# Performance work log

Hardware: AMD Instinct MI355X
Metric: run time of the kernel (lower is better)

## Reference

```python
import jax, jax.numpy as jnp
import numpy as np

T_ITERS = 10
EPS = 1e-5


def setup_inputs() -> dict:
    key = jax.random.key(0)
    B, C, H, W = 64, 256, 56, 56
    X = jax.random.normal(key, (B, C, H, W), dtype=jnp.float32)
    # running_rot buffer: orthogonal rotation per group (g=1)
    M = np.random.default_rng(0).standard_normal((C, C)).astype(np.float32)
    q, _ = np.linalg.qr(M)
    running_rot = jnp.asarray(q[None, :, :])  # [g=1, d, d]
    return {"X": X, "running_rot": running_rot}


def _whiten(X, g, nc):
    # X: [B, C, H, W] -> x: [g, d, m] with m = B*H*W (training-mode IterNorm)
    B, C, H, W = X.shape
    x = jnp.transpose(X, (1, 0, 2, 3)).reshape(g, nc, -1)
    m = x.shape[-1]
    mean = jnp.mean(x, axis=-1, keepdims=True)          # [g, d, 1]
    xc = x - mean                                        # [g, d, m]
    I = jnp.broadcast_to(jnp.eye(nc, dtype=X.dtype), (g, nc, nc))
    Sigma = EPS * I + jnp.matmul(xc, jnp.swapaxes(xc, 1, 2)) * (1.0 / m)
    # rTr = 1 / trace(Sigma) per group
    rTr = 1.0 / jnp.sum(Sigma * I, axis=(1, 2), keepdims=True)  # [g,1,1]
    Sigma_N = Sigma * rTr
    # Newton-Schulz iteration: P_{k+1} = 1.5 P_k - 0.5 P_k^3 Sigma_N
    P = I
    for _ in range(T_ITERS):
        P3 = jnp.matmul(jnp.matmul(P, P), P)
        P = 1.5 * P - 0.5 * jnp.matmul(P3, Sigma_N)
    wm = P * jnp.sqrt(rTr)                               # whitening matrix [g,d,d]
    xn = jnp.matmul(wm, xc)                              # [g, d, m]
    return xn.reshape(C, B, H, W).transpose(1, 0, 2, 3)  # back to [B,C,H,W]


def reference(X, running_rot):
    g, _, nc = running_rot.shape
    B, C, H, W = X.shape
    X_hat = _whiten(X, g, nc)                            # [B, C, H, W]
    Xg = X_hat.reshape(B, g, nc, H, W)
    # rotate whitened features: Q^T alignment, einsum('bgchw,gdc->bgdhw')
    Xr = jnp.einsum('bgchw,gdc->bgdhw', Xg, running_rot)
    return Xr.reshape(B, C, H, W)
```

## Files before the change

### kernel.cpp

```cpp
#include <hip/hip_runtime.h>
#include <math.h>

#define HWn   3136
#define Cn    256
#define KCPB  49
#define NCHUNK 3136
#define INV_M (1.0f/200704.0f)
#define EPSc  1e-5f

typedef __attribute__((ext_vector_type(4))) float f32x4;
typedef __attribute__((ext_vector_type(8))) short s16x8;
typedef __attribute__((ext_vector_type(4))) unsigned short u16x4;

static __device__ __forceinline__ unsigned short f2bf(float f) {
  unsigned int u = __builtin_bit_cast(unsigned int, f);
  u = (u + 0x7fffu + ((u >> 16) & 1u)) >> 16;
  return (unsigned short)u;
}

static __device__ __forceinline__ unsigned int cvt_pk_bf16(float lo, float hi) {
  unsigned int r;
  asm("v_cvt_pk_bf16_f32 %0, %1, %2" : "=v"(r) : "v"(lo), "v"(hi));
  return r;
}

__global__ __launch_bounds__(1024) void k_gram(const float* __restrict__ X,
                                               float* __restrict__ Gp,
                                               float* __restrict__ Sp,
                                               float* __restrict__ Dp,
                                               int nparts) {
  __shared__ __align__(16) unsigned short lds[2][256 * 64];
  const int t = threadIdx.x, p = blockIdx.x;
  const int w = t >> 6, l = t & 63, a = l & 15, g = l >> 4;
  const int swzA = (a & 7) << 3;
  const int crow = t >> 4, sg = t & 15;

  f32x4 acc[16];
#pragma unroll
  for (int j = 0; j < 16; ++j) acc[j] = (f32x4){0.f, 0.f, 0.f, 0.f};
  float sum4[4] = {0.f, 0.f, 0.f, 0.f};
  float vx[16];

  const int start = (int)(((long)NCHUNK * p) / nparts);
  const int end   = (int)(((long)NCHUNK * (p + 1)) / nparts);

#define G_LOADS(CH)                                                           \
  {                                                                           \
    const int b_ = (CH) / KCPB, kc_ = (CH) % KCPB;                            \
    const float* xb_ = X + (long)b_ * Cn * HWn + kc_ * 64;                    \
    _Pragma("unroll")                                                         \
    for (int p4 = 0; p4 < 4; ++p4) {                                          \
      const float4 v = *(const float4*)(xb_ + (long)(p4 * 64 + crow) * HWn + sg * 4); \
      vx[p4 * 4 + 0] = v.x; vx[p4 * 4 + 1] = v.y;                             \
      vx[p4 * 4 + 2] = v.z; vx[p4 * 4 + 3] = v.w;                             \
    }                                                                         \
  }

#define G_CVTWR(BUF)                                                          \
  {                                                                           \
    _Pragma("unroll")                                                         \
    for (int p4 = 0; p4 < 4; ++p4) {                                          \
      const int c_ = p4 * 64 + crow;                                          \
      sum4[p4] += (vx[p4 * 4 + 0] + vx[p4 * 4 + 1])                           \
                + (vx[p4 * 4 + 2] + vx[p4 * 4 + 3]);                          \
      uint2 hh;                                                               \
      hh.x = cvt_pk_bf16(vx[p4 * 4 + 0], vx[p4 * 4 + 1]);                     \
      hh.y = cvt_pk_bf16(vx[p4 * 4 + 2], vx[p4 * 4 + 3]);                     \
      *(uint2*)(&lds[BUF][0] + ((c_ * 64 + sg * 4) ^ ((c_ & 7) << 3))) = hh;  \
    }                                                                         \
  }

  G_LOADS(start);
  G_CVTWR(0);
  __syncthreads();

  for (int ch = start; ch < end; ++ch) {
    const int cur = (ch - start) & 1;
    if (ch + 1 < end) G_LOADS(ch + 1);
    const unsigned short* tile = &lds[cur][0];
#pragma unroll
    for (int kk = 0; kk < 64; kk += 32) {
      const s16x8 fw = *(const s16x8*)(tile + (((w * 16 + a) * 64 + kk + g * 8) ^ swzA));
#pragma unroll
      for (int j = 0; j < 16; ++j) {
        const s16x8 fj = *(const s16x8*)(tile + (((j * 16 + a) * 64 + kk + g * 8) ^ swzA));
        acc[j] = __builtin_amdgcn_mfma_f32_16x16x32_bf16(fw, fj, acc[j], 0, 0, 0);
      }
    }
    if (ch + 1 < end) G_CVTWR(cur ^ 1);
    __syncthreads();
  }
#undef G_LOADS
#undef G_CVTWR

  float* gout = Gp + (long)p * 65536;
#pragma unroll
  for (int j = 0; j < 16; ++j)
#pragma unroll
    for (int r = 0; r < 4; ++r)
      __builtin_nontemporal_store(acc[j][r],
          gout + (16 * w + 4 * g + r) * 256 + 16 * j + a);

#pragma unroll
  for (int p4 = 0; p4 < 4; ++p4) {
    float s = sum4[p4];
    s += __shfl_xor(s, 1);
    s += __shfl_xor(s, 2);
    s += __shfl_xor(s, 4);
    s += __shfl_xor(s, 8);
    if (a == 0) Sp[(long)p * 256 + p4 * 64 + w * 4 + g] = s;
  }

  {
    float dsum = 0.f;
#pragma unroll
    for (int j = 0; j < 16; ++j) {
      if (j == w && (a >> 2) == g) {
#pragma unroll
        for (int r = 0; r < 4; ++r)
          if ((a & 3) == r) dsum = acc[j][r];
      }
    }
#pragma unroll
    for (int off = 1; off < 64; off <<= 1) dsum += __shfl_xor(dsum, off);
    float* lf = (float*)lds;
    if (l == 0) lf[w] = dsum;
    __syncthreads();
    if (t == 0) {
      float d = 0.f;
#pragma unroll
      for (int ww = 0; ww < 16; ++ww) d += lf[ww];
      Dp[p] = d;
    }
  }
}

__global__ __launch_bounds__(1024) void k_reduce(const float* __restrict__ Gp,
                                                 const float* __restrict__ Sp,
                                                 const float* __restrict__ Dp,
                                                 float* __restrict__ Sigma,
                                                 float* __restrict__ P1,
                                                 float* __restrict__ meansum,
                                                 float* __restrict__ scal,
                                                 int nparts) {
  __shared__ float redA[4][256];
  __shared__ float msh[256];
  __shared__ float scrD[256];
  __shared__ float scrM[256];
  __shared__ __align__(16) float redB[16][256];
  const int t = threadIdx.x, j = blockIdx.x;
  const int c = t & 255, g = t >> 8;

  {
    float s = 0.f;
    const int pa0 = (nparts * g) >> 2, pa1 = (nparts * (g + 1)) >> 2;
    for (int p = pa0; p < pa1; ++p) s += Sp[(long)p * 256 + c];
    redA[g][c] = s;
  }
  __syncthreads();
  if (g == 0) msh[c] = (redA[0][c] + redA[1][c]) + (redA[2][c] + redA[3][c]);
  __syncthreads();

  if (t < 256) {
    scrD[t] = (t < nparts) ? Dp[t] : 0.f;
    const float mc = msh[t] * INV_M;
    scrM[t] = mc * mc;
  }
  __syncthreads();
  for (int st = 128; st > 0; st >>= 1) {
    if (t < st) { scrD[t] += scrD[t + st]; scrM[t] += scrM[t + st]; }
    __syncthreads();
  }
  const float tr = scrD[0] * INV_M - scrM[0] + 256.f * EPSc;
  const float rTr = 1.0f / tr;

  {
    const int c4 = (t & 63) * 4, sl = t >> 6;
    const int pb0 = (nparts * sl) >> 4, pb1 = (nparts * (sl + 1)) >> 4;
    const float* gp = Gp + (long)pb0 * 65536 + (long)j * 256 + c4;
    f32x4 s4 = (f32x4){0.f, 0.f, 0.f, 0.f};
    for (int p = pb0; p < pb1; ++p) {
      s4 += __builtin_nontemporal_load((const f32x4*)gp);
      gp += 65536;
    }
    *(f32x4*)&redB[sl][c4] = s4;
  }
  __syncthreads();

  if (t < 256) {
    float t0 = 0.f, t1 = 0.f;
#pragma unroll
    for (int sl = 0; sl < 16; sl += 2) { t0 += redB[sl][t]; t1 += redB[sl + 1][t]; }
    const float tot = t0 + t1;
    const float mc = msh[t] * INV_M;
    const float mj = msh[j] * INV_M;
    const float sig = tot * INV_M - mj * mc + ((j == t) ? EPSc : 0.f);
    Sigma[(long)j * 256 + t] = sig;
    P1[(long)j * 256 + t] = ((j == t) ? 1.5f : 0.f) - 0.5f * rTr * sig;
    if (j == 0) {
      meansum[t] = msh[t];
      if (t == 0) { scal[0] = tr; scal[1] = rTr; scal[2] = sqrtf(rTr); }
    }
  }
}

__global__ __launch_bounds__(1024) void k_ns(const float* __restrict__ Ps,
                                             float* __restrict__ Pd,
                                             const float* __restrict__ Sig,
                                             const float* __restrict__ scal) {
  __shared__ __align__(16) float PT[256][4];
  __shared__ __align__(16) float red[4][256][4];
  const int t = threadIdx.x, c = t & 255, kh = t >> 8, k0 = kh * 64;
  const int r0 = blockIdx.x * 4;

  PT[c][kh] = Ps[(r0 + kh) * 256 + c];
  __syncthreads();

  f32x4 acc;

#define NS_PHASE(BPTR)                                                        \
  {                                                                           \
    acc = (f32x4){0.f, 0.f, 0.f, 0.f};                                        \
    const float* Bb = (BPTR) + (long)k0 * 256 + c;                            \
    _Pragma("unroll 8")                                                       \
    for (int kk = 0; kk < 64; ++kk) {                                         \
      const float b = Bb[(long)kk * 256];                                     \
      const f32x4 a4 = *(const f32x4*)&PT[k0 + kk][0];                        \
      acc += a4 * b;                                                          \
    }                                                                         \
    *(f32x4*)&red[kh][c][0] = acc;                                            \
    __syncthreads();                                                          \
  }

#define NS_COMBINE()                                                          \
  {                                                                           \
    const f32x4 vs = (*(const f32x4*)&red[0][c][0] + *(const f32x4*)&red[1][c][0]) \
                   + (*(const f32x4*)&red[2][c][0] + *(const f32x4*)&red[3][c][0]); \
    if (kh == 0) *(f32x4*)&PT[c][0] = vs;                                     \
    __syncthreads();                                                          \
  }

  NS_PHASE(Ps);
  NS_COMBINE();
  NS_PHASE(Ps);
  NS_COMBINE();
  NS_PHASE(Sig);

  const float rTr = scal[1];
  const float t3 = ((red[0][c][kh] + red[1][c][kh]) + (red[2][c][kh] + red[3][c][kh]));
  const float pr = Ps[(r0 + kh) * 256 + c];
  Pd[(r0 + kh) * 256 + c] = 1.5f * pr - 0.5f * rTr * t3;
}

__global__ __launch_bounds__(1024) void k_ns_makeA(const float* __restrict__ Ps,
                                                   const float* __restrict__ Sig,
                                                   const float* __restrict__ rot,
                                                   const float* __restrict__ scal,
                                                   const float* __restrict__ meansum,
                                                   unsigned short* __restrict__ Abf,
                                                   float* __restrict__ bias) {
  __shared__ __align__(16) float PT[256][4];
  __shared__ __align__(16) float red[4][256][4];
  __shared__ float Tw[4][256];
  const int t = threadIdx.x, c = t & 255, kh = t >> 8, k0 = kh * 64;
  const int r0 = blockIdx.x * 4;

  PT[c][kh] = rot[(r0 + kh) * 256 + c];
  __syncthreads();

  f32x4 acc;

  NS_PHASE(Ps);
  NS_COMBINE();
  const float t1 = PT[c][kh];
  NS_PHASE(Ps);
  NS_COMBINE();
  NS_PHASE(Ps);
  NS_COMBINE();
  NS_PHASE(Sig);

  const float rTr = scal[1];
  const float sq = scal[2];
  const float t4 = (red[0][c][kh] + red[1][c][kh]) + (red[2][c][kh] + red[3][c][kh]);
  const float av = sq * (1.5f * t1 - 0.5f * rTr * t4);
  Abf[(r0 + kh) * 256 + c] = f2bf(av);
  const float mc = meansum[c] * INV_M;
  Tw[kh][c] = av * mc;
  __syncthreads();
  for (int st = 128; st > 0; st >>= 1) {
    if (c < st) Tw[kh][c] += Tw[kh][c + st];
    __syncthreads();
  }
  if (c == 0) bias[r0 + kh] = Tw[kh][0];
#undef NS_PHASE
#undef NS_COMBINE
}

__global__ __launch_bounds__(1024) void k_apply(const float* __restrict__ X,
                                                const unsigned short* __restrict__ Abf,
                                                const float* __restrict__ bias,
                                                float* __restrict__ out) {
  __shared__ __align__(16) unsigned short lds[2][64 * 256];
  const int t = threadIdx.x, w = t >> 6, l = t & 63, a = l & 15, g = l >> 4;
  const int bid = blockIdx.x;
  const int b = bid >> 3, strip = bid & 7;
  const int ch0 = (49 * strip) >> 3, ch1 = (49 * (strip + 1)) >> 3;

  const int d = 16 * w + a;
  s16x8 af[8];
#pragma unroll
  for (int kk8 = 0; kk8 < 8; ++kk8)
    af[kk8] = *(const s16x8*)(Abf + d * 256 + kk8 * 32 + g * 8);
  const float bd = bias[d];

  const float* xbase = X + (long)b * Cn * HWn;
  float* obase = out + (long)b * Cn * HWn;
  float vx[16];

#define A_LOADS(CH)                                                           \
  {                                                                           \
    const int s0_ = (CH) * 64;                                                \
    _Pragma("unroll")                                                         \
    for (int p4 = 0; p4 < 4; ++p4) {                                          \
      const int c4_ = p4 * 16 + w;                                            \
      const float* xp_ = xbase + (long)(c4_ * 4) * HWn + s0_ + l;             \
      vx[p4 * 4 + 0] = xp_[0];                                                \
      vx[p4 * 4 + 1] = xp_[HWn];                                              \
      vx[p4 * 4 + 2] = xp_[2 * HWn];                                          \
      vx[p4 * 4 + 3] = xp_[3 * HWn];                                          \
    }                                                                         \
  }

#define A_CVTWR(BUF)                                                          \
  {                                                                           \
    _Pragma("unroll")                                                         \
    for (int p4 = 0; p4 < 4; ++p4) {                                          \
      const int c4_ = p4 * 16 + w;                                            \
      uint2 hh;                                                               \
      hh.x = cvt_pk_bf16(vx[p4 * 4 + 0], vx[p4 * 4 + 1]);                     \
      hh.y = cvt_pk_bf16(vx[p4 * 4 + 2], vx[p4 * 4 + 3]);                     \
      *(uint2*)(&lds[BUF][0] + ((l * 256 + c4_ * 4) ^ ((l & 7) << 3))) = hh;  \
    }                                                                         \
  }

  A_LOADS(ch0);
  A_CVTWR(0);
  __syncthreads();

  for (int ch = ch0; ch < ch1; ++ch) {
    const int cur = (ch - ch0) & 1;
    if (ch + 1 < ch1) A_LOADS(ch + 1);

    const unsigned short* tile = &lds[cur][0];
    f32x4 acc[4];
#pragma unroll
    for (int st = 0; st < 4; ++st) acc[st] = (f32x4){0.f, 0.f, 0.f, 0.f};
#pragma unroll
    for (int kk8 = 0; kk8 < 8; ++kk8) {
#pragma unroll
      for (int st = 0; st < 4; ++st) {
        const s16x8 xf = *(const s16x8*)(tile + (((st * 16 + a) * 256 + kk8 * 32 + g * 8) ^ ((a & 7) << 3)));
        acc[st] = __builtin_amdgcn_mfma_f32_16x16x32_bf16(xf, af[kk8], acc[st], 0, 0, 0);
      }
    }
    const int s0 = ch * 64;
#pragma unroll
    for (int st = 0; st < 4; ++st) {
      const f32x4 o = acc[st] - bd;
      __builtin_nontemporal_store(o, (f32x4*)(obase + (long)d * HWn + s0 + st * 16 + 4 * g));
    }

    if (ch + 1 < ch1) A_CVTWR(cur ^ 1);
    __syncthreads();
  }
#undef A_LOADS
#undef A_CVTWR
}

extern "C" void kernel_launch(void* const* d_in, const int* in_sizes, int n_in,
                              void* d_out, int out_size, void* d_ws, size_t ws_size,
                              hipStream_t stream) {
  const float* X = (const float*)d_in[0];
  const float* rot = (const float*)d_in[1];
  float* out = (float*)d_out;

  auto need = [](int np) -> size_t {
    return (size_t)4 * ((size_t)np * 65536 + (size_t)np * 256 + (size_t)np
                        + 3 * 65536 + 256 + 16 + 256)
         + (size_t)2 * 65536;
  };
  int nparts = 128;
  while (nparts > 4 && need(nparts) > ws_size) nparts >>= 1;

  float* w = (float*)d_ws;
  float* Gp = w;       w += (size_t)nparts * 65536;
  float* Sp = w;       w += (size_t)nparts * 256;
  float* Dp = w;       w += (size_t)nparts;
  float* Sigma = w;    w += 65536;
  float* P0 = w;       w += 65536;
  float* P1 = w;       w += 65536;
  float* meansum = w;  w += 256;
  float* scal = w;     w += 16;
  float* bias = w;     w += 256;
  unsigned short* Abf = (unsigned short*)w;

  k_gram<<<dim3(nparts), dim3(1024), 0, stream>>>(X, Gp, Sp, Dp, nparts);
  k_reduce<<<dim3(256), dim3(1024), 0, stream>>>(Gp, Sp, Dp, Sigma, P1, meansum, scal, nparts);
  float* ps = P1;
  float* pd = P0;
  for (int i = 0; i < 8; ++i) {
    k_ns<<<dim3(64), dim3(1024), 0, stream>>>(ps, pd, Sigma, scal);
    float* tmp = ps; ps = pd; pd = tmp;
  }
  k_ns_makeA<<<dim3(64), dim3(1024), 0, stream>>>(ps, Sigma, rot, scal, meansum, Abf, bias);
  k_apply<<<dim3(512), dim3(1024), 0, stream>>>(X, Abf, bias, out);
}
```

Measured before the change: 285.0 us.

## Restructure gram kernel to 512 threads with 32-row warp tiles and 256 partitions

The Gram kernel now runs 8 waves per block, each computing 32 rows of the 256x256 product. Each wave loads two A fragments and reuses every B fragment for four MFMAs, which halves the LDS reads per MFMA. The global loads change from 16 threads per channel row to 2 threads per row with eight float4 loads each. The partition count doubles to 256 to fill the GPU, at the cost of more partial Gram matrices for k_reduce to read and higher register pressure from 128 accumulators per thread.

```diff
diff --git a/kernel.cpp b/kernel.cpp
--- a/kernel.cpp
+++ b/kernel.cpp
@@ -24,22 +24,24 @@
   return r;
 }
 
-__global__ __launch_bounds__(1024) void k_gram(const float* __restrict__ X,
-                                               float* __restrict__ Gp,
-                                               float* __restrict__ Sp,
-                                               float* __restrict__ Dp,
-                                               int nparts) {
+__global__ __launch_bounds__(512) void k_gram(const float* __restrict__ X,
+                                              float* __restrict__ Gp,
+                                              float* __restrict__ Sp,
+                                              float* __restrict__ Dp,
+                                              int nparts) {
   __shared__ __align__(16) unsigned short lds[2][256 * 64];
   const int t = threadIdx.x, p = blockIdx.x;
   const int w = t >> 6, l = t & 63, a = l & 15, g = l >> 4;
   const int swzA = (a & 7) << 3;
-  const int crow = t >> 4, sg = t & 15;
-
-  f32x4 acc[16];
-#pragma unroll
-  for (int j = 0; j < 16; ++j) acc[j] = (f32x4){0.f, 0.f, 0.f, 0.f};
-  float sum4[4] = {0.f, 0.f, 0.f, 0.f};
-  float vx[16];
+  const int crow = t >> 1, h = t & 1;
+
+  f32x4 acc[2][16];
+#pragma unroll
+  for (int rb = 0; rb < 2; ++rb)
+#pragma unroll
+    for (int j = 0; j < 16; ++j) acc[rb][j] = (f32x4){0.f, 0.f, 0.f, 0.f};
+  float sumc = 0.f;
+  float vx[32];
 
   const int start = (int)(((long)NCHUNK * p) / nparts);
   const int end   = (int)(((long)NCHUNK * (p + 1)) / nparts);
@@ -47,27 +49,29 @@
 #define G_LOADS(CH)                                                           \
   {                                                                           \
     const int b_ = (CH) / KCPB, kc_ = (CH) % KCPB;                            \
-    const float* xb_ = X + (long)b_ * Cn * HWn + kc_ * 64;                    \
+    const float* xb_ = X + (long)b_ * Cn * HWn + kc_ * 64                     \
+                         + (long)crow * HWn + h * 32;                         \
     _Pragma("unroll")                                                         \
-    for (int p4 = 0; p4 < 4; ++p4) {                                          \
-      const float4 v = *(const float4*)(xb_ + (long)(p4 * 64 + crow) * HWn + sg * 4); \
-      vx[p4 * 4 + 0] = v.x; vx[p4 * 4 + 1] = v.y;                             \
-      vx[p4 * 4 + 2] = v.z; vx[p4 * 4 + 3] = v.w;                             \
+    for (int q = 0; q < 8; ++q) {                                             \
+      const float4 v = *(const float4*)(xb_ + q * 4);                         \
+      vx[q * 4 + 0] = v.x; vx[q * 4 + 1] = v.y;                               \
+      vx[q * 4 + 2] = v.z; vx[q * 4 + 3] = v.w;                               \
     }                                                                         \
   }
 
 #define G_CVTWR(BUF)                                                          \
   {                                                                           \
+    float s_ = 0.f;                                                           \
     _Pragma("unroll")                                                         \
-    for (int p4 = 0; p4 < 4; ++p4) {                                          \
-      const int c_ = p4 * 64 + crow;                                          \
-      sum4[p4] += (vx[p4 * 4 + 0] + vx[p4 * 4 + 1])                           \
-                + (vx[p4 * 4 + 2] + vx[p4 * 4 + 3]);                          \
+    for (int q = 0; q < 8; ++q) {                                             \
+      s_ += (vx[q * 4 + 0] + vx[q * 4 + 1]) + (vx[q * 4 + 2] + vx[q * 4 + 3]); \
       uint2 hh;                                                               \
-      hh.x = cvt_pk_bf16(vx[p4 * 4 + 0], vx[p4 * 4 + 1]);                     \
-      hh.y = cvt_pk_bf16(vx[p4 * 4 + 2], vx[p4 * 4 + 3]);                     \
-      *(uint2*)(&lds[BUF][0] + ((c_ * 64 + sg * 4) ^ ((c_ & 7) << 3))) = hh;  \
+      hh.x = cvt_pk_bf16(vx[q * 4 + 0], vx[q * 4 + 1]);                       \
+      hh.y = cvt_pk_bf16(vx[q * 4 + 2], vx[q * 4 + 3]);                       \
+      *(uint2*)(&lds[BUF][0] +                                                \
+          ((crow * 64 + h * 32 + q * 4) ^ ((crow & 7) << 3))) = hh;           \
     }                                                                         \
+    sumc += s_;                                                               \
   }
 
   G_LOADS(start);
@@ -78,14 +82,21 @@
     const int cur = (ch - start) & 1;
     if (ch + 1 < end) G_LOADS(ch + 1);
     const unsigned short* tile = &lds[cur][0];
-#pragma unroll
-    for (int kk = 0; kk < 64; kk += 32) {
-      const s16x8 fw = *(const s16x8*)(tile + (((w * 16 + a) * 64 + kk + g * 8) ^ swzA));
-#pragma unroll
-      for (int j = 0; j < 16; ++j) {
-        const s16x8 fj = *(const s16x8*)(tile + (((j * 16 + a) * 64 + kk + g * 8) ^ swzA));
-        acc[j] = __builtin_amdgcn_mfma_f32_16x16x32_bf16(fw, fj, acc[j], 0, 0, 0);
-      }
+    s16x8 fw[2][2];
+#pragma unroll
+    for (int rb = 0; rb < 2; ++rb)
+#pragma unroll
+      for (int kk2 = 0; kk2 < 2; ++kk2)
+        fw[rb][kk2] = *(const s16x8*)(tile +
+            ((((2 * w + rb) * 16 + a) * 64 + kk2 * 32 + g * 8) ^ swzA));
+#pragma unroll
+    for (int j = 0; j < 16; ++j) {
+      const s16x8 fj0 = *(const s16x8*)(tile + (((j * 16 + a) * 64 + 0  + g * 8) ^ swzA));
+      const s16x8 fj1 = *(const s16x8*)(tile + (((j * 16 + a) * 64 + 32 + g * 8) ^ swzA));
+      acc[0][j] = __builtin_amdgcn_mfma_f32_16x16x32_bf16(fw[0][0], fj0, acc[0][j], 0, 0, 0);
+      acc[0][j] = __builtin_amdgcn_mfma_f32_16x16x32_bf16(fw[0][1], fj1, acc[0][j], 0, 0, 0);
+      acc[1][j] = __builtin_amdgcn_mfma_f32_16x16x32_bf16(fw[1][0], fj0, acc[1][j], 0, 0, 0);
+      acc[1][j] = __builtin_amdgcn_mfma_f32_16x16x32_bf16(fw[1][1], fj1, acc[1][j], 0, 0, 0);
     }
     if (ch + 1 < end) G_CVTWR(cur ^ 1);
     __syncthreads();
@@ -95,41 +106,39 @@
 
   float* gout = Gp + (long)p * 65536;
 #pragma unroll
-  for (int j = 0; j < 16; ++j)
-#pragma unroll
-    for (int r = 0; r < 4; ++r)
-      __builtin_nontemporal_store(acc[j][r],
-          gout + (16 * w + 4 * g + r) * 256 + 16 * j + a);
-
-#pragma unroll
-  for (int p4 = 0; p4 < 4; ++p4) {
-    float s = sum4[p4];
-    s += __shfl_xor(s, 1);
-    s += __shfl_xor(s, 2);
-    s += __shfl_xor(s, 4);
-    s += __shfl_xor(s, 8);
-    if (a == 0) Sp[(long)p * 256 + p4 * 64 + w * 4 + g] = s;
+  for (int rb = 0; rb < 2; ++rb)
+#pragma unroll
+    for (int j = 0; j < 16; ++j)
+#pragma unroll
+      for (int r = 0; r < 4; ++r)
+        __builtin_nontemporal_store(acc[rb][j][r],
+            gout + (32 * w + 16 * rb + 4 * g + r) * 256 + 16 * j + a);
+
+  {
+    const float so = __shfl_xor(sumc, 1);
+    if ((t & 1) == 0) Sp[(long)p * 256 + crow] = sumc + so;
   }
 
   {
     float dsum = 0.f;
 #pragma unroll
-    for (int j = 0; j < 16; ++j) {
-      if (j == w && (a >> 2) == g) {
-#pragma unroll
-        for (int r = 0; r < 4; ++r)
-          if ((a & 3) == r) dsum = acc[j][r];
-      }
-    }
+    for (int rb = 0; rb < 2; ++rb)
+#pragma unroll
+      for (int jj = 0; jj < 16; ++jj)
+        if (jj == 2 * w + rb)
+#pragma unroll
+          for (int r = 0; r < 4; ++r)
+            if (a == 4 * g + r) dsum += acc[rb][jj][r];
 #pragma unroll
     for (int off = 1; off < 64; off <<= 1) dsum += __shfl_xor(dsum, off);
     float* lf = (float*)lds;
+    __syncthreads();
     if (l == 0) lf[w] = dsum;
     __syncthreads();
     if (t == 0) {
       float d = 0.f;
 #pragma unroll
-      for (int ww = 0; ww < 16; ++ww) d += lf[ww];
+      for (int ww = 0; ww < 8; ++ww) d += lf[ww];
       Dp[p] = d;
     }
   }
@@ -389,7 +398,7 @@
                         + 3 * 65536 + 256 + 16 + 256)
          + (size_t)2 * 65536;
   };
-  int nparts = 128;
+  int nparts = 256;
   while (nparts > 4 && need(nparts) > ws_size) nparts >>= 1;
 
   float* w = (float*)d_ws;
@@ -404,7 +413,7 @@
   float* bias = w;     w += 256;
   unsigned short* Abf = (unsigned short*)w;
 
-  k_gram<<<dim3(nparts), dim3(1024), 0, stream>>>(X, Gp, Sp, Dp, nparts);
+  k_gram<<<dim3(nparts), dim3(512), 0, stream>>>(X, Gp, Sp, Dp, nparts);
   k_reduce<<<dim3(256), dim3(1024), 0, stream>>>(Gp, Sp, Dp, Sigma, P1, meansum, scal, nparts);
   float* ps = P1;
   float* pd = P0;
```

New measurement: 277.6 us. 2.6% less time.
